# Kernel tuning notes

Measured on AMD Instinct MI355X. Metric: run time of the kernel, lower is better.

The kernel has to match this reference:

```python
import jax, jax.numpy as jnp
import numpy as np

B, N, D, H = 128, 2048, 128, 8
HD = D // H


def setup_inputs() -> dict:
    key = jax.random.key(0)
    ks = jax.random.split(key, 10)
    x = jax.random.normal(ks[0], (B, N, D), dtype=jnp.float32)
    first_node = jax.random.randint(ks[1], (B, 1), 0, N, dtype=jnp.int64)
    current_node = jax.random.randint(ks[2], (B, 1), 0, N, dtype=jnp.int64)
    mask = jax.random.randint(ks[3], (B, N), 0, 2).astype(jnp.bool_)
    s = 0.02
    W_lin = jax.random.normal(ks[4], (D, 3 * D), dtype=jnp.float32) * s
    b_lin = jnp.zeros((D,), dtype=jnp.float32)
    Wq = jax.random.normal(ks[5], (D, D), dtype=jnp.float32) * s
    bq = jnp.zeros((D,), dtype=jnp.float32)
    Wk = jax.random.normal(ks[6], (D, D), dtype=jnp.float32) * s
    bk = jnp.zeros((D,), dtype=jnp.float32)
    return {"x": x, "first_node": first_node, "current_node": current_node,
            "mask": mask, "W_lin": W_lin, "b_lin": b_lin,
            "Wq": Wq, "bq": bq, "Wk": Wk, "bk": bk}


def reference(x, first_node, current_node, mask, W_lin, b_lin, Wq, bq, Wk, bk):
    # y = x.clone().detach()
    y = jax.lax.stop_gradient(x)
    graph_emb = jnp.mean(y, axis=-2)                       # [B, D]
    bidx = jnp.arange(B)
    first_feat = y[bidx, first_node[:, 0]]                 # [B, D]
    curr_feat = y[bidx, current_node[:, 0]]                # [B, D]
    context = jnp.concatenate([graph_emb, first_feat, curr_feat], axis=-1)  # [B, 3D]
    q_in = context @ W_lin.T + b_lin                       # [B, D]
    # single-query multi-head attention; only attn weights are used
    q = (q_in @ Wq.T + bq).reshape(B, H, HD)               # [B, H, hd]
    k = (x @ Wk.T + bk).reshape(B, N, H, HD)               # [B, N, H, hd]
    scores = jnp.einsum('bhd,bnhd->bhn', q, k) / jnp.sqrt(jnp.float32(HD))
    scores = jnp.where(mask[:, None, :], -jnp.inf, scores)  # key_padding_mask: True = masked
    attn = jax.nn.softmax(scores, axis=-1)                 # [B, H, N]
    return jnp.mean(attn, axis=1)                          # average over heads -> [B, N]
```

## Files before the change

kernel.cpp:

```cpp
#include <hip/hip_runtime.h>
#include <hip/hip_bf16.h>

#define BB 128
#define NN 2048
#define DD 128
#define HH 8

#define GSP_OFF  0
#define WQE_OFF  131072
#define SB_OFF   262144
#define ESP_OFF  263168
#define E_OFF    271360

__launch_bounds__(256)
__global__ void k1_gsum(const float* __restrict__ x, float* __restrict__ gsp) {
    int b = blockIdx.y, cx = blockIdx.x, t = threadIdx.x;
    int c4 = t & 31, rg = t >> 5;
    const float4* x4 = (const float4*)(x + ((size_t)b * NN + cx * 256) * DD);
    float4 acc = make_float4(0.f, 0.f, 0.f, 0.f);
    #pragma unroll 8
    for (int i = 0; i < 32; ++i) {
        float4 v = x4[(size_t)(rg + 8 * i) * 32 + c4];
        acc.x += v.x; acc.y += v.y; acc.z += v.z; acc.w += v.w;
    }
    acc.x += __shfl_xor(acc.x, 32, 64);
    acc.y += __shfl_xor(acc.y, 32, 64);
    acc.z += __shfl_xor(acc.z, 32, 64);
    acc.w += __shfl_xor(acc.w, 32, 64);
    __shared__ float xsum[4][32][4];
    int w = t >> 6, lane = t & 63;
    if (lane < 32) {
        xsum[w][lane][0] = acc.x; xsum[w][lane][1] = acc.y;
        xsum[w][lane][2] = acc.z; xsum[w][lane][3] = acc.w;
    }
    __syncthreads();
    if (t < 32) {
        float4 s;
        s.x = xsum[0][t][0] + xsum[1][t][0] + xsum[2][t][0] + xsum[3][t][0];
        s.y = xsum[0][t][1] + xsum[1][t][1] + xsum[2][t][1] + xsum[3][t][1];
        s.z = xsum[0][t][2] + xsum[1][t][2] + xsum[2][t][2] + xsum[3][t][2];
        s.w = xsum[0][t][3] + xsum[1][t][3] + xsum[2][t][3] + xsum[3][t][3];
        ((float4*)(gsp + ((size_t)b * 8 + cx) * 128))[t] = s;
    }
}

__launch_bounds__(256)
__global__ void k2(const float* __restrict__ x,
                   const int* __restrict__ fn_p, const int* __restrict__ cn_p,
                   const float* __restrict__ Wl, const float* __restrict__ bl,
                   const float* __restrict__ Wq, const float* __restrict__ bq,
                   const float* __restrict__ Wk, const float* __restrict__ bk,
                   float* ws) {
    __shared__ float ctxL[384];
    __shared__ float qpart[2][128];
    __shared__ float qinL[128];
    __shared__ float qvL[128];
    int b = blockIdx.x, t = threadIdx.x;
    bool is64 = (fn_p[1] == 0 && fn_p[3] == 0 && fn_p[5] == 0 && fn_p[7] == 0 &&
                 cn_p[1] == 0 && cn_p[3] == 0 && cn_p[5] == 0 && cn_p[7] == 0);
    int fn = is64 ? fn_p[2 * b] : fn_p[b];
    int cn = is64 ? cn_p[2 * b] : cn_p[b];

    const float* gsp = ws + GSP_OFF + (size_t)b * 8 * 128;
    if (t < 128) {
        float g = 0.f;
        #pragma unroll
        for (int i = 0; i < 8; ++i) g += gsp[i * 128 + t];
        ctxL[t]       = g * (1.0f / NN);
        ctxL[256 + t] = x[((size_t)b * NN + cn) * DD + t];
    } else {
        int u = t - 128;
        ctxL[128 + u] = x[((size_t)b * NN + fn) * DD + u];
    }
    __syncthreads();

    int m = t & 127, half = t >> 7;
    {
        const float* wrow = Wl + (size_t)m * 384 + half * 192;
        const float* cp = ctxL + half * 192;
        float part = 0.f;
        #pragma unroll 8
        for (int e = 0; e < 192; ++e) part = fmaf(wrow[e], cp[e], part);
        qpart[half][m] = part;
    }
    __syncthreads();
    if (t < 128) qinL[t] = qpart[0][t] + qpart[1][t] + bl[t];
    __syncthreads();

    {
        const float* wrow = Wq + (size_t)m * 128 + half * 64;
        const float* cp = qinL + half * 64;
        float part = 0.f;
        #pragma unroll 8
        for (int c = 0; c < 64; ++c) part = fmaf(wrow[c], cp[c], part);
        qpart[half][m] = part;
    }
    __syncthreads();
    if (t < 128) qvL[t] = qpart[0][t] + qpart[1][t] + bq[t];
    __syncthreads();

    float* wqe = ws + WQE_OFF + (size_t)b * (HH * DD);
    #pragma unroll
    for (int i = t; i < 1024; i += 256) {
        int h = i >> 7, d = i & 127;
        float s = 0.f;
        #pragma unroll
        for (int j = 0; j < 16; ++j)
            s = fmaf(qvL[h * 16 + j], Wk[(size_t)(h * 16 + j) * 128 + d], s);
        wqe[i] = 0.25f * s;
    }
    if (t < HH) {
        float s = 0.f;
        #pragma unroll
        for (int j = 0; j < 16; ++j) s = fmaf(qvL[t * 16 + j], bk[t * 16 + j], s);
        (ws + SB_OFF)[b * HH + t] = 0.25f * s;
    }
}

__device__ __forceinline__ int detect_mask_kind(const int* mw) {
    int big = 0, oddnz = 0;
    #pragma unroll 8
    for (int i = 0; i < 64; ++i) {
        unsigned w = (unsigned)mw[i];
        if (w > 1u) big = 1;
        if ((i & 1) && w != 0u) oddnz = 1;
    }
    return big ? 0 : (oddnz ? 1 : 2);
}
__device__ __forceinline__ int mask_at(const unsigned char* mb, const int* mw, int kind, size_t idx) {
    if (kind == 0) return mb[idx];
    if (kind == 1) return mw[idx];
    return mw[2 * idx];
}

__global__ void k3(const float* __restrict__ x, const void* __restrict__ mask,
                   const float* __restrict__ ws_ro,
                   float* __restrict__ wse, float* __restrict__ esp) {
    __shared__ float4 wq4[256];
    __shared__ float sbL[8];
    __shared__ float ps[4][8];
    int b = blockIdx.y, cx = blockIdx.x, t = threadIdx.x;
    const float4* wqe4 = (const float4*)(ws_ro + WQE_OFF + (size_t)b * 1024);
    wq4[t] = wqe4[t];
    if (t < 8) sbL[t] = (ws_ro + SB_OFF)[b * HH + t];
    __syncthreads();

    const unsigned char* mb = (const unsigned char*)mask;
    const int* mw = (const int*)mask;
    int mkind = detect_mask_kind(mw);

    int n = cx * 256 + t;
    const float4* xr = (const float4*)(x + ((size_t)b * NN + n) * DD);

    float acc[HH];
    #pragma unroll
    for (int h = 0; h < HH; ++h) acc[h] = sbL[h];

    #pragma unroll 4
    for (int q = 0; q < 32; ++q) {
        float4 v = xr[q];
        #pragma unroll
        for (int h = 0; h < HH; ++h) {
            float4 w = wq4[h * 32 + q];
            acc[h] = fmaf(v.x, w.x, fmaf(v.y, w.y, fmaf(v.z, w.z, fmaf(v.w, w.w, acc[h]))));
        }
    }

    int msk = mask_at(mb, mw, mkind, (size_t)b * NN + n);
    float ev[HH];
    #pragma unroll
    for (int h = 0; h < HH; ++h) ev[h] = msk ? 0.f : __expf(acc[h]);

    float4 E0 = make_float4(ev[0], ev[1], ev[2], ev[3]);
    float4 E1 = make_float4(ev[4], ev[5], ev[6], ev[7]);
    float4* wp = (float4*)(wse + ((size_t)b * NN + n) * 8);
    wp[0] = E0; wp[1] = E1;

    int w = t >> 6, lane = t & 63;
    #pragma unroll
    for (int h = 0; h < HH; ++h) {
        float v = ev[h];
        #pragma unroll
        for (int off = 32; off >= 1; off >>= 1) v += __shfl_xor(v, off, 64);
        if (lane == 0) ps[w][h] = v;
    }
    __syncthreads();
    if (t < 8)
        esp[((size_t)b * 8 + cx) * 8 + t] = ps[0][t] + ps[1][t] + ps[2][t] + ps[3][t];
}

__global__ void k4_out(const float* __restrict__ wse, const float* __restrict__ esp,
                       float* __restrict__ out) {
    __shared__ float rinv[8];
    int b = blockIdx.y, cx = blockIdx.x, t = threadIdx.x;
    if (t < 8) {
        float s = 0.f;
        #pragma unroll
        for (int i = 0; i < 8; ++i) s += esp[((size_t)b * 8 + i) * 8 + t];
        rinv[t] = 0.125f / s;
    }
    __syncthreads();
    int n = cx * 256 + t;
    const float4* ep = (const float4*)(wse + ((size_t)b * NN + n) * 8);
    float4 e0 = ep[0], e1 = ep[1];
    out[(size_t)b * NN + n] =
        e0.x * rinv[0] + e0.y * rinv[1] + e0.z * rinv[2] + e0.w * rinv[3] +
        e1.x * rinv[4] + e1.y * rinv[5] + e1.z * rinv[6] + e1.w * rinv[7];
}

extern "C" void kernel_launch(void* const* d_in, const int* in_sizes, int n_in,
                              void* d_out, int out_size, void* d_ws, size_t ws_size,
                              hipStream_t stream) {
    const float* x  = (const float*)d_in[0];
    const int* fn   = (const int*)d_in[1];
    const int* cn   = (const int*)d_in[2];
    const void* mk  = d_in[3];
    const float* Wl = (const float*)d_in[4];
    const float* bl = (const float*)d_in[5];
    const float* Wq = (const float*)d_in[6];
    const float* bq = (const float*)d_in[7];
    const float* Wk = (const float*)d_in[8];
    const float* bk = (const float*)d_in[9];
    float* ws  = (float*)d_ws;
    float* out = (float*)d_out;

    k1_gsum<<<dim3(8, BB), 256, 0, stream>>>(x, ws + GSP_OFF);
    k2<<<BB, 256, 0, stream>>>(x, fn, cn, Wl, bl, Wq, bq, Wk, bk, ws);
    k3<<<dim3(8, BB), 256, 0, stream>>>(x, mk, ws, ws + E_OFF, ws + ESP_OFF);
    k4_out<<<dim3(8, BB), 256, 0, stream>>>(ws + E_OFF, ws + ESP_OFF, out);
}
```

Before: 259.5 us.

## Batch four queries per k2 block with LDS-tiled weight staging

k2 now handles four batch rows per block, 32 blocks instead of 128. The Wl and Wq matvecs stage 32-column weight tiles into padded LDS so each thread reuses a weight across two batch rows. The Wk projection reuses each Wk load across all four rows. This cuts redundant weight traffic, whose uncoalesced per-thread row reads were slow, but it lowers parallelism to 32 blocks on a GPU with many CUs.

```diff
diff --git a/kernel.cpp b/kernel.cpp
--- a/kernel.cpp
+++ b/kernel.cpp
@@ -47,73 +47,110 @@
 __launch_bounds__(256)
 __global__ void k2(const float* __restrict__ x,
                    const int* __restrict__ fn_p, const int* __restrict__ cn_p,
-                   const float* __restrict__ Wl, const float* __restrict__ bl,
-                   const float* __restrict__ Wq, const float* __restrict__ bq,
-                   const float* __restrict__ Wk, const float* __restrict__ bk,
+                   const float* __restrict__ Wl, const float* __restrict__ blv,
+                   const float* __restrict__ Wq, const float* __restrict__ bqv,
+                   const float* __restrict__ Wk, const float* __restrict__ bkv,
                    float* ws) {
-    __shared__ float ctxL[384];
-    __shared__ float qpart[2][128];
-    __shared__ float qinL[128];
-    __shared__ float qvL[128];
-    int b = blockIdx.x, t = threadIdx.x;
+    __shared__ float ctxL[4][384];
+    __shared__ float wT[128 * 33];
+    __shared__ float qinL[4][128];
+    __shared__ float qvL[4][128];
+    int b0 = blockIdx.x * 4, t = threadIdx.x;
+
     bool is64 = (fn_p[1] == 0 && fn_p[3] == 0 && fn_p[5] == 0 && fn_p[7] == 0 &&
                  cn_p[1] == 0 && cn_p[3] == 0 && cn_p[5] == 0 && cn_p[7] == 0);
-    int fn = is64 ? fn_p[2 * b] : fn_p[b];
-    int cn = is64 ? cn_p[2 * b] : cn_p[b];
-
-    const float* gsp = ws + GSP_OFF + (size_t)b * 8 * 128;
-    if (t < 128) {
-        float g = 0.f;
-        #pragma unroll
-        for (int i = 0; i < 8; ++i) g += gsp[i * 128 + t];
-        ctxL[t]       = g * (1.0f / NN);
-        ctxL[256 + t] = x[((size_t)b * NN + cn) * DD + t];
-    } else {
-        int u = t - 128;
-        ctxL[128 + u] = x[((size_t)b * NN + fn) * DD + u];
-    }
-    __syncthreads();
-
-    int m = t & 127, half = t >> 7;
+
+    #pragma unroll
+    for (int q = 0; q < 4; ++q) {
+        int b = b0 + q;
+        int fn = is64 ? fn_p[2 * b] : fn_p[b];
+        int cn = is64 ? cn_p[2 * b] : cn_p[b];
+        const float* gsp = ws + GSP_OFF + (size_t)b * 1024;
+        if (t < 128) {
+            float g = 0.f;
+            #pragma unroll
+            for (int i = 0; i < 8; ++i) g += gsp[i * 128 + t];
+            ctxL[q][t]       = g * (1.0f / NN);
+            ctxL[q][256 + t] = x[((size_t)b * NN + cn) * DD + t];
+        } else {
+            int u = t - 128;
+            ctxL[q][128 + u] = x[((size_t)b * NN + fn) * DD + u];
+        }
+    }
+
+    int m = t & 127, pair = t >> 7;
+    int bA = 2 * pair, bC = 2 * pair + 1;
+
+    float acc0 = 0.f, acc1 = 0.f;
+    for (int tile = 0; tile < 12; ++tile) {
+        int e0 = tile * 32;
+        __syncthreads();
+        #pragma unroll
+        for (int k = 0; k < 16; ++k) {
+            int idx = t + k * 256, r = idx >> 5, c = idx & 31;
+            wT[r * 33 + c] = Wl[(size_t)r * 384 + e0 + c];
+        }
+        __syncthreads();
+        #pragma unroll 8
+        for (int e = 0; e < 32; ++e) {
+            float w = wT[m * 33 + e];
+            acc0 = fmaf(w, ctxL[bA][e0 + e], acc0);
+            acc1 = fmaf(w, ctxL[bC][e0 + e], acc1);
+        }
+    }
     {
-        const float* wrow = Wl + (size_t)m * 384 + half * 192;
-        const float* cp = ctxL + half * 192;
-        float part = 0.f;
+        float bb = blv[m];
+        qinL[bA][m] = acc0 + bb;
+        qinL[bC][m] = acc1 + bb;
+    }
+
+    acc0 = 0.f; acc1 = 0.f;
+    for (int tile = 0; tile < 4; ++tile) {
+        int c0 = tile * 32;
+        __syncthreads();
+        #pragma unroll
+        for (int k = 0; k < 16; ++k) {
+            int idx = t + k * 256, r = idx >> 5, c = idx & 31;
+            wT[r * 33 + c] = Wq[(size_t)r * 128 + c0 + c];
+        }
+        __syncthreads();
         #pragma unroll 8
-        for (int e = 0; e < 192; ++e) part = fmaf(wrow[e], cp[e], part);
-        qpart[half][m] = part;
-    }
-    __syncthreads();
-    if (t < 128) qinL[t] = qpart[0][t] + qpart[1][t] + bl[t];
-    __syncthreads();
-
+        for (int c = 0; c < 32; ++c) {
+            float w = wT[m * 33 + c];
+            acc0 = fmaf(w, qinL[bA][c0 + c], acc0);
+            acc1 = fmaf(w, qinL[bC][c0 + c], acc1);
+        }
+    }
     {
-        const float* wrow = Wq + (size_t)m * 128 + half * 64;
-        const float* cp = qinL + half * 64;
-        float part = 0.f;
-        #pragma unroll 8
-        for (int c = 0; c < 64; ++c) part = fmaf(wrow[c], cp[c], part);
-        qpart[half][m] = part;
-    }
-    __syncthreads();
-    if (t < 128) qvL[t] = qpart[0][t] + qpart[1][t] + bq[t];
-    __syncthreads();
-
-    float* wqe = ws + WQE_OFF + (size_t)b * (HH * DD);
-    #pragma unroll
-    for (int i = t; i < 1024; i += 256) {
-        int h = i >> 7, d = i & 127;
+        float bb = bqv[m];
+        qvL[bA][m] = acc0 + bb;
+        qvL[bC][m] = acc1 + bb;
+    }
+    __syncthreads();
+
+    #pragma unroll
+    for (int i4 = 0; i4 < 4; ++i4) {
+        int i = t + i4 * 256, h = i >> 7, d = i & 127;
+        float s0 = 0.f, s1 = 0.f, s2 = 0.f, s3 = 0.f;
+        #pragma unroll
+        for (int j = 0; j < 16; ++j) {
+            float w = Wk[(size_t)(h * 16 + j) * 128 + d];
+            s0 = fmaf(qvL[0][h * 16 + j], w, s0);
+            s1 = fmaf(qvL[1][h * 16 + j], w, s1);
+            s2 = fmaf(qvL[2][h * 16 + j], w, s2);
+            s3 = fmaf(qvL[3][h * 16 + j], w, s3);
+        }
+        ws[WQE_OFF + (size_t)(b0 + 0) * 1024 + i] = 0.25f * s0;
+        ws[WQE_OFF + (size_t)(b0 + 1) * 1024 + i] = 0.25f * s1;
+        ws[WQE_OFF + (size_t)(b0 + 2) * 1024 + i] = 0.25f * s2;
+        ws[WQE_OFF + (size_t)(b0 + 3) * 1024 + i] = 0.25f * s3;
+    }
+    if (t < 32) {
+        int bl_ = t >> 3, h = t & 7;
         float s = 0.f;
         #pragma unroll
-        for (int j = 0; j < 16; ++j)
-            s = fmaf(qvL[h * 16 + j], Wk[(size_t)(h * 16 + j) * 128 + d], s);
-        wqe[i] = 0.25f * s;
-    }
-    if (t < HH) {
-        float s = 0.f;
-        #pragma unroll
-        for (int j = 0; j < 16; ++j) s = fmaf(qvL[t * 16 + j], bk[t * 16 + j], s);
-        (ws + SB_OFF)[b * HH + t] = 0.25f * s;
+        for (int j = 0; j < 16; ++j) s = fmaf(qvL[bl_][h * 16 + j], bkv[h * 16 + j], s);
+        (ws + SB_OFF)[(b0 + bl_) * HH + h] = 0.25f * s;
     }
 }
 
@@ -225,7 +262,7 @@
     float* out = (float*)d_out;
 
     k1_gsum<<<dim3(8, BB), 256, 0, stream>>>(x, ws + GSP_OFF);
-    k2<<<BB, 256, 0, stream>>>(x, fn, cn, Wl, bl, Wq, bq, Wk, bk, ws);
+    k2<<<32, 256, 0, stream>>>(x, fn, cn, Wl, bl, Wq, bq, Wk, bk, ws);
     k3<<<dim3(8, BB), 256, 0, stream>>>(x, mk, ws, ws + E_OFF, ws + ESP_OFF);
     k4_out<<<dim3(8, BB), 256, 0, stream>>>(ws + E_OFF, ws + ESP_OFF, out);
 }
```

Measured after the change: 271.5 us. +4.6%, slower.
